# Kernel tuning notes

Measured on AMD Instinct MI355X. Metric: run time of the kernel, lower is better.

## Reference

```python
import jax, jax.numpy as jnp
import numpy as np

B, N, IN_F, OUT_F, REL_DIM, NUM_REL = 4, 2048, 256, 128, 10, 6
D = OUT_F // 2  # internal_dim
ALPHA = 0.2
LAMBDA_INIT = 0.8 - 0.6 * float(np.exp(-0.3 * 1))  # depth=1
EPS = 1e-5


def setup_inputs() -> dict:
    key = jax.random.key(0)
    ks = jax.random.split(key, 16)
    return {
        "h": jax.random.normal(ks[0], (B, N, IN_F), jnp.float32),
        "adj": jax.random.randint(ks[1], (B, N, N), 0, NUM_REL, jnp.int32),
        "W": jax.random.normal(ks[2], (IN_F, OUT_F), jnp.float32) * (1.414 / np.sqrt(IN_F)),
        "a_left_pos": jax.random.normal(ks[3], (D,), jnp.float32) * 0.1,
        "a_right_pos": jax.random.normal(ks[4], (D,), jnp.float32) * 0.1,
        "a_left_neg": jax.random.normal(ks[5], (D,), jnp.float32) * 0.1,
        "a_right_neg": jax.random.normal(ks[6], (D,), jnp.float32) * 0.1,
        "rel_emb": jax.random.normal(ks[7], (NUM_REL, REL_DIM), jnp.float32),
        "a_rel_pos": jax.random.normal(ks[8], (REL_DIM,), jnp.float32) * 0.3,
        "a_rel_neg": jax.random.normal(ks[9], (REL_DIM,), jnp.float32) * 0.3,
        "lambda_left1": jax.random.normal(ks[10], (D,), jnp.float32) * 0.1,
        "lambda_right1": jax.random.normal(ks[11], (D,), jnp.float32) * 0.1,
        "lambda_left2": jax.random.normal(ks[12], (D,), jnp.float32) * 0.1,
        "lambda_right2": jax.random.normal(ks[13], (D,), jnp.float32) * 0.1,
        "ln_gamma": jnp.ones((OUT_F,), jnp.float32),
        "ln_beta": jnp.zeros((OUT_F,), jnp.float32),
    }


def _leaky_relu(x):
    return jnp.where(x >= 0, x, ALPHA * x)


def reference(h, adj, W, a_left_pos, a_right_pos, a_left_neg, a_right_neg,
              rel_emb, a_rel_pos, a_rel_neg,
              lambda_left1, lambda_right1, lambda_left2, lambda_right2,
              ln_gamma, ln_beta):
    Wh = jnp.einsum('bnf,fo->bno', h, W)              # [B,N,OUT_F]
    Wh4 = Wh.reshape(B, N, 2, D)
    Wh_pos, Wh_neg = Wh4[:, :, 0, :], Wh4[:, :, 1, :]  # [B,N,D]

    # e[b,i,j] = left[b,i] + right[b,j] + rel_score[adj[b,i,j]]
    # relation Linear(rel_dim,1) applied to embedding rows == per-relation scalar lookup
    rel_score_pos = rel_emb @ a_rel_pos               # [NUM_REL]
    rel_score_neg = rel_emb @ a_rel_neg
    e_pos = (Wh_pos @ a_left_pos)[:, :, None] + (Wh_pos @ a_right_pos)[:, None, :] + rel_score_pos[adj]
    e_neg = (Wh_neg @ a_left_neg)[:, :, None] + (Wh_neg @ a_right_neg)[:, None, :] + rel_score_neg[adj]

    neg_inf = jnp.float32(-9e15)
    mask = adj > 0
    attn_pos = jax.nn.softmax(jnp.where(mask, _leaky_relu(e_pos), neg_inf), axis=2)
    attn_neg = jax.nn.softmax(jnp.where(mask, _leaky_relu(e_neg), neg_inf), axis=2)

    lam1 = jnp.exp(jnp.sum(lambda_left1 * lambda_right1))
    lam2 = jnp.exp(jnp.sum(lambda_left2 * lambda_right2))
    lambda_full = lam1 - lam2 + LAMBDA_INIT
    attention = attn_pos - lambda_full * attn_neg     # [B,N,N]

    Wh_v = jnp.concatenate([Wh_pos, Wh_neg], axis=-1)  # [B,N,OUT_F]
    h_prime = jnp.einsum('bij,bjo->bio', attention, Wh_v)

    mu = jnp.mean(h_prime, axis=-1, keepdims=True)
    var = jnp.mean(jnp.square(h_prime - mu), axis=-1, keepdims=True)
    h_prime = (h_prime - mu) * jax.lax.rsqrt(var + EPS) * ln_gamma + ln_beta
    h_prime = h_prime * (1.0 - LAMBDA_INIT)
    return jax.nn.gelu(h_prime, approximate=False), attention
```

## Files before the change

### kernel.cpp

```cpp
#include <hip/hip_runtime.h>
#include <math.h>

typedef short bf16x8 __attribute__((ext_vector_type(8)));
typedef float f32x4  __attribute__((ext_vector_type(4)));

constexpr int   B_    = 4;
constexpr int   N_    = 2048;
constexpr int   INF_  = 256;
constexpr int   OUTF_ = 128;
constexpr float LAMBDA_INIT_ = 0.35550906759096926f;
constexpr float OUT_SCALE_   = 0.64449093240903074f;
constexpr float EPS_         = 1e-5f;
constexpr float LOG2E_       = 1.44269504088896340736f;

__device__ inline unsigned short f2bf(float x) {
  unsigned u = __float_as_uint(x);
  u += 0x7fffu + ((u >> 16) & 1u);
  return (unsigned short)(u >> 16);
}
__device__ inline unsigned pack2(float a, float b) {
  return (unsigned)f2bf(a) | ((unsigned)f2bf(b) << 16);
}

__global__ void scalars_kernel(const float* __restrict__ rel_emb,
                               const float* __restrict__ a_rel_pos,
                               const float* __restrict__ a_rel_neg,
                               const float* __restrict__ ll1, const float* __restrict__ lr1,
                               const float* __restrict__ ll2, const float* __restrict__ lr2,
                               float* __restrict__ scal) {
  int lane = threadIdx.x;
  float p1 = ll1[lane] * lr1[lane];
  float p2 = ll2[lane] * lr2[lane];
  #pragma unroll
  for (int off = 32; off; off >>= 1) { p1 += __shfl_xor(p1, off); p2 += __shfl_xor(p2, off); }
  if (lane == 0) scal[12] = expf(p1) - expf(p2) + LAMBDA_INIT_;
  if (lane < 6) {
    float sp = 0.f, sn = 0.f;
    for (int k = 0; k < 10; ++k) {
      float rv = rel_emb[lane * 10 + k];
      sp += rv * a_rel_pos[k];
      sn += rv * a_rel_neg[k];
    }
    scal[lane]     = sp * LOG2E_;
    scal[6 + lane] = sn * LOG2E_;
  }
}

__global__ __launch_bounds__(256) void wh_dots_kernel(
    const float* __restrict__ h, const float* __restrict__ W,
    const float* __restrict__ alp, const float* __restrict__ arp,
    const float* __restrict__ aln, const float* __restrict__ arn,
    unsigned short* __restrict__ WhvT,
    float* __restrict__ lposv, float* __restrict__ rposv,
    float* __restrict__ lnegv, float* __restrict__ rnegv) {
  __shared__ __align__(16) float hT[INF_][20];
  const int t = threadIdx.x;
  const size_t row0 = (size_t)blockIdx.x * 16;
  #pragma unroll
  for (int i = 0; i < 16; ++i) hT[t][i] = h[(row0 + i) * INF_ + t];
  __syncthreads();
  const int c  = t & 127;
  const int rg = t >> 7;
  float acc[8] = {0.f, 0.f, 0.f, 0.f, 0.f, 0.f, 0.f, 0.f};
  #pragma unroll 4
  for (int k = 0; k < INF_; ++k) {
    float wv = W[k * OUTF_ + c];
    const float4* hp = reinterpret_cast<const float4*>(&hT[k][rg * 8]);
    float4 h0 = hp[0], h1 = hp[1];
    acc[0] += h0.x * wv; acc[1] += h0.y * wv; acc[2] += h0.z * wv; acc[3] += h0.w * wv;
    acc[4] += h1.x * wv; acc[5] += h1.y * wv; acc[6] += h1.z * wv; acc[7] += h1.w * wv;
  }
  uint4 pk;
  pk.x = pack2(acc[0], acc[1]); pk.y = pack2(acc[2], acc[3]);
  pk.z = pack2(acc[4], acc[5]); pk.w = pack2(acc[6], acc[7]);
  const int b  = (int)(row0 >> 11);
  const int n0 = (int)(row0 & 2047) + rg * 8;
  *reinterpret_cast<uint4*>(WhvT + ((size_t)b * OUTF_ + c) * N_ + n0) = pk;

  const int lane = t & 63;
  const int wv   = t >> 6;
  const bool pos = (wv & 1) == 0;
  const float al = pos ? alp[lane] : aln[lane];
  const float ar = pos ? arp[lane] : arn[lane];
  float sl[8], sr2[8];
  #pragma unroll
  for (int r = 0; r < 8; ++r) { sl[r] = acc[r] * al; sr2[r] = acc[r] * ar; }
  #pragma unroll
  for (int off = 32; off; off >>= 1) {
    #pragma unroll
    for (int r = 0; r < 8; ++r) {
      sl[r]  += __shfl_xor(sl[r],  off);
      sr2[r] += __shfl_xor(sr2[r], off);
    }
  }
  if (lane == 0) {
    #pragma unroll
    for (int r = 0; r < 8; ++r) {
      const int node = (int)row0 + rg * 8 + r;
      if (pos) { lposv[node] = sl[r] * LOG2E_; rposv[node] = sr2[r] * LOG2E_; }
      else     { lnegv[node] = sl[r] * LOG2E_; rnegv[node] = sr2[r] * LOG2E_; }
    }
  }
}

__global__ __launch_bounds__(512, 4) void fused_attn_pv(
    const int* __restrict__ adj,
    const float* __restrict__ lposv, const float* __restrict__ rposv,
    const float* __restrict__ lnegv, const float* __restrict__ rnegv,
    const float* __restrict__ scal, const unsigned short* __restrict__ WhvT,
    const float* __restrict__ gamma, const float* __restrict__ beta,
    float* __restrict__ out0, float* __restrict__ out1) {
  __shared__ __align__(16) uint4 A4[16 * 256];
  float* scr = reinterpret_cast<float*>(&A4[15 * 256]);
  float (*hp)[132] = reinterpret_cast<float (*)[132]>(A4);

  const int t = threadIdx.x;
  const int lane = t & 63;
  const int wv = t >> 6;
  const int bi = blockIdx.x;
  const int b  = bi >> 7;
  const int i0 = (bi & 127) * 16;
  const int flat0 = b * N_ + i0;

  const float lam = scal[12];
  float srcP = -1.0e30f, srcN = -1.0e30f;
  if (lane >= 1 && lane <= 5) { srcP = scal[lane]; srcN = scal[6 + lane]; }
  const int iSrcP = __float_as_int(srcP);
  const int iSrcN = __float_as_int(srcN);

  const int j0 = t * 4;
  float4 rp4 = *reinterpret_cast<const float4*>(rposv + b * N_ + j0);
  float4 rn4 = *reinterpret_cast<const float4*>(rnegv + b * N_ + j0);
  const float rp[4] = {rp4.x, rp4.y, rp4.z, rp4.w};
  const float rn[4] = {rn4.x, rn4.y, rn4.z, rn4.w};

  const int wchunk = (t >> 1) >> 5;
  const int wloc   = (t >> 1) & 31;

  int4 avN = *reinterpret_cast<const int4*>(adj + (size_t)flat0 * N_ + j0);

  for (int r = 0; r < 16; ++r) {
    const int flat = flat0 + r;
    const int4 av4 = avN;
    if (r < 15)
      avN = *reinterpret_cast<const int4*>(adj + (size_t)(flat + 1) * N_ + j0);
    const float lP = lposv[flat];
    const float lN = lnegv[flat];
    int av[4] = {av4.x, av4.y, av4.z, av4.w};

    float p[4], n[4];
    #pragma unroll
    for (int q = 0; q < 4; ++q) {
      float rsp = __int_as_float(__builtin_amdgcn_ds_bpermute(av[q] << 2, iSrcP));
      float rsn = __int_as_float(__builtin_amdgcn_ds_bpermute(av[q] << 2, iSrcN));
      float e  = lP + rp[q] + rsp;
      float en = lN + rn[q] + rsn;
      e  = fmaxf(e, 0.2f * e);
      en = fmaxf(en, 0.2f * en);
      p[q] = __builtin_amdgcn_exp2f(e);
      n[q] = __builtin_amdgcn_exp2f(en);
    }
    float sP = (p[0] + p[1]) + (p[2] + p[3]);
    float sN = (n[0] + n[1]) + (n[2] + n[3]);
    #pragma unroll
    for (int off = 32; off; off >>= 1) { sP += __shfl_xor(sP, off); sN += __shfl_xor(sN, off); }
    const int bf = r & 1;
    if (lane == 0) { scr[bf * 16 + wv] = sP; scr[bf * 16 + 8 + wv] = sN; }
    __syncthreads();
    float vP = scr[bf * 16 + (lane & 7)];
    vP += __shfl_xor(vP, 1); vP += __shfl_xor(vP, 2); vP += __shfl_xor(vP, 4);
    float vN = scr[bf * 16 + 8 + (lane & 7)];
    vN += __shfl_xor(vN, 1); vN += __shfl_xor(vN, 2); vN += __shfl_xor(vN, 4);
    const float s1 = 1.f / vP;
    const float s2 = -lam / vN;

    float a[4];
    #pragma unroll
    for (int q = 0; q < 4; ++q) a[q] = p[q] * s1 + n[q] * s2;
    float* o1 = out1 + (size_t)flat * N_ + j0;
    *reinterpret_cast<float4*>(o1) = make_float4(a[0], a[1], a[2], a[3]);

    if (r == 15) __syncthreads();
    const int uidx = r * 256 + wchunk * 32 + (wloc ^ (r & 7));
    uint2 val;
    val.x = pack2(a[0], a[1]); val.y = pack2(a[2], a[3]);
    reinterpret_cast<uint2*>(A4)[uidx * 2 + (t & 1)] = val;
  }
  __syncthreads();

  const int bl  = lane & 15;
  const int kg  = lane >> 4;
  const int ch  = wv * 16 + bl;
  const unsigned short* Bp = WhvT + ((size_t)b * OUTF_ + ch) * N_ + kg * 8;
  f32x4 acc0 = {0.f, 0.f, 0.f, 0.f};
  f32x4 acc1 = {0.f, 0.f, 0.f, 0.f};
  const int arow = bl * 256;
  const int aswz = bl & 7;

  bf16x8 bBuf[2][8];
  #pragma unroll
  for (int kk = 0; kk < 8; ++kk)
    bBuf[0][kk] = *reinterpret_cast<const bf16x8*>(Bp + kk * 32);

  #pragma unroll
  for (int c = 0; c < 8; ++c) {
    const int cur = c & 1;
    if (c < 7) {
      #pragma unroll
      for (int kk = 0; kk < 8; ++kk)
        bBuf[cur ^ 1][kk] = *reinterpret_cast<const bf16x8*>(Bp + (c + 1) * 256 + kk * 32);
    }
    #pragma unroll
    for (int kk = 0; kk < 8; ++kk) {
      bf16x8 a = *reinterpret_cast<const bf16x8*>(&A4[arow + c * 32 + ((kk * 4 + kg) ^ aswz)]);
      if (cur == 0) acc0 = __builtin_amdgcn_mfma_f32_16x16x32_bf16(a, bBuf[0][kk], acc0, 0, 0, 0);
      else          acc1 = __builtin_amdgcn_mfma_f32_16x16x32_bf16(a, bBuf[1][kk], acc1, 0, 0, 0);
    }
  }
  __syncthreads();

  #pragma unroll
  for (int q = 0; q < 4; ++q) hp[kg * 4 + q][ch] = acc0[q] + acc1[q];
  __syncthreads();

  const int row = t >> 5;
  const int c0  = t & 31;
  float v[4], s = 0.f, sq = 0.f;
  #pragma unroll
  for (int e = 0; e < 4; ++e) {
    v[e] = hp[row][c0 + e * 32];
    s += v[e]; sq += v[e] * v[e];
  }
  #pragma unroll
  for (int off = 16; off; off >>= 1) { s += __shfl_xor(s, off); sq += __shfl_xor(sq, off); }
  const float mu  = s  * (1.f / 128.f);
  const float var = sq * (1.f / 128.f) - mu * mu;
  const float inv = rsqrtf(var + EPS_);
  float* orow = out0 + ((size_t)(b * N_ + i0 + row)) * OUTF_;
  #pragma unroll
  for (int e = 0; e < 4; ++e) {
    const int chh = c0 + e * 32;
    float y = (v[e] - mu) * inv * gamma[chh] + beta[chh];
    y *= OUT_SCALE_;
    orow[chh] = 0.5f * y * (1.f + erff(y * 0.70710678118654752f));
  }
}

extern "C" void kernel_launch(void* const* d_in, const int* in_sizes, int n_in,
                              void* d_out, int out_size, void* d_ws, size_t ws_size,
                              hipStream_t stream) {
  (void)in_sizes; (void)n_in; (void)out_size; (void)ws_size;
  const float* h        = (const float*)d_in[0];
  const int*   adj      = (const int*)d_in[1];
  const float* W        = (const float*)d_in[2];
  const float* alp      = (const float*)d_in[3];
  const float* arp      = (const float*)d_in[4];
  const float* aln      = (const float*)d_in[5];
  const float* arn      = (const float*)d_in[6];
  const float* rel_emb  = (const float*)d_in[7];
  const float* a_rel_p  = (const float*)d_in[8];
  const float* a_rel_n  = (const float*)d_in[9];
  const float* ll1      = (const float*)d_in[10];
  const float* lr1      = (const float*)d_in[11];
  const float* ll2      = (const float*)d_in[12];
  const float* lr2      = (const float*)d_in[13];
  const float* gamma    = (const float*)d_in[14];
  const float* beta     = (const float*)d_in[15];

  float* out0 = (float*)d_out;
  float* out1 = out0 + (size_t)B_ * N_ * OUTF_;

  float* ws    = (float*)d_ws;
  float* scal  = ws;
  float* lposv = ws + 32;
  float* rposv = lposv + B_ * N_;
  float* lnegv = rposv + B_ * N_;
  float* rnegv = lnegv + B_ * N_;
  unsigned short* WhvT = (unsigned short*)(rnegv + B_ * N_);

  scalars_kernel<<<1, 64, 0, stream>>>(rel_emb, a_rel_p, a_rel_n, ll1, lr1, ll2, lr2, scal);
  wh_dots_kernel<<<(B_ * N_) / 16, 256, 0, stream>>>(h, W, alp, arp, aln, arn,
                                                     WhvT, lposv, rposv, lnegv, rnegv);
  fused_attn_pv<<<B_ * (N_ / 16), 512, 0, stream>>>(adj, lposv, rposv, lnegv, rnegv,
                                                    scal, WhvT, gamma, beta, out0, out1);
}
```

Before: 89.39 us.

## Retile Wh projection kernel to 4x4 register blocking over 32-row tiles

Rewrites the h·W projection kernel so each block handles 32 rows and each thread computes a 4-row by 4-column register tile, loading W and h as float4 vectors. This raises arithmetic intensity and cuts per-FMA shared-memory and global load traffic compared with the previous one-column, eight-row scheme. The attention-vector dot products are now reduced over 16-lane groups rather than full waves. The grid is halved, so fewer blocks are available to fill the GPU, and the kernel is a small part of total time next to the attention kernel.

Measured after the change: 81.97 us. 1.09x faster.

```diff
diff --git a/kernel.cpp b/kernel.cpp
--- a/kernel.cpp
+++ b/kernel.cpp
@@ -46,59 +46,93 @@
   }
 }
 
-__global__ __launch_bounds__(256) void wh_dots_kernel(
+__global__ __launch_bounds__(256) void wh_dots_v2(
     const float* __restrict__ h, const float* __restrict__ W,
     const float* __restrict__ alp, const float* __restrict__ arp,
     const float* __restrict__ aln, const float* __restrict__ arn,
     unsigned short* __restrict__ WhvT,
     float* __restrict__ lposv, float* __restrict__ rposv,
     float* __restrict__ lnegv, float* __restrict__ rnegv) {
-  __shared__ __align__(16) float hT[INF_][20];
+  __shared__ __align__(16) float hT[32][260];
   const int t = threadIdx.x;
-  const size_t row0 = (size_t)blockIdx.x * 16;
-  #pragma unroll
-  for (int i = 0; i < 16; ++i) hT[t][i] = h[(row0 + i) * INF_ + t];
+  const int row0 = blockIdx.x * 32;
+  const int b = row0 >> 11;
+
+  #pragma unroll 8
+  for (int i = 0; i < 32; ++i) hT[i][t] = h[(size_t)(row0 + i) * INF_ + t];
   __syncthreads();
-  const int c  = t & 127;
-  const int rg = t >> 7;
-  float acc[8] = {0.f, 0.f, 0.f, 0.f, 0.f, 0.f, 0.f, 0.f};
-  #pragma unroll 4
-  for (int k = 0; k < INF_; ++k) {
-    float wv = W[k * OUTF_ + c];
-    const float4* hp = reinterpret_cast<const float4*>(&hT[k][rg * 8]);
-    float4 h0 = hp[0], h1 = hp[1];
-    acc[0] += h0.x * wv; acc[1] += h0.y * wv; acc[2] += h0.z * wv; acc[3] += h0.w * wv;
-    acc[4] += h1.x * wv; acc[5] += h1.y * wv; acc[6] += h1.z * wv; acc[7] += h1.w * wv;
-  }
-  uint4 pk;
-  pk.x = pack2(acc[0], acc[1]); pk.y = pack2(acc[2], acc[3]);
-  pk.z = pack2(acc[4], acc[5]); pk.w = pack2(acc[6], acc[7]);
-  const int b  = (int)(row0 >> 11);
-  const int n0 = (int)(row0 & 2047) + rg * 8;
-  *reinterpret_cast<uint4*>(WhvT + ((size_t)b * OUTF_ + c) * N_ + n0) = pk;
-
-  const int lane = t & 63;
-  const int wv   = t >> 6;
-  const bool pos = (wv & 1) == 0;
-  const float al = pos ? alp[lane] : aln[lane];
-  const float ar = pos ? arp[lane] : arn[lane];
-  float sl[8], sr2[8];
-  #pragma unroll
-  for (int r = 0; r < 8; ++r) { sl[r] = acc[r] * al; sr2[r] = acc[r] * ar; }
-  #pragma unroll
-  for (int off = 32; off; off >>= 1) {
-    #pragma unroll
-    for (int r = 0; r < 8; ++r) {
-      sl[r]  += __shfl_xor(sl[r],  off);
-      sr2[r] += __shfl_xor(sr2[r], off);
-    }
-  }
-  if (lane == 0) {
-    #pragma unroll
-    for (int r = 0; r < 8; ++r) {
-      const int node = (int)row0 + rg * 8 + r;
-      if (pos) { lposv[node] = sl[r] * LOG2E_; rposv[node] = sr2[r] * LOG2E_; }
-      else     { lnegv[node] = sl[r] * LOG2E_; rnegv[node] = sr2[r] * LOG2E_; }
+
+  const int rg = t >> 5;
+  const int cg = t & 31;
+  const int c0 = cg * 4;
+  float acc[4][4] = {{0.f,0.f,0.f,0.f},{0.f,0.f,0.f,0.f},{0.f,0.f,0.f,0.f},{0.f,0.f,0.f,0.f}};
+
+  #pragma unroll 2
+  for (int k4 = 0; k4 < 64; ++k4) {
+    float4 hv[4], wv[4];
+    #pragma unroll
+    for (int rr = 0; rr < 4; ++rr)
+      hv[rr] = *reinterpret_cast<const float4*>(&hT[rg * 4 + rr][k4 * 4]);
+    #pragma unroll
+    for (int j = 0; j < 4; ++j)
+      wv[j] = *reinterpret_cast<const float4*>(&W[(size_t)(k4 * 4 + j) * OUTF_ + c0]);
+    #pragma unroll
+    for (int rr = 0; rr < 4; ++rr) {
+      const float* hp = reinterpret_cast<const float*>(&hv[rr]);
+      #pragma unroll
+      for (int j = 0; j < 4; ++j) {
+        const float* wp = reinterpret_cast<const float*>(&wv[j]);
+        acc[rr][0] += hp[j] * wp[0];
+        acc[rr][1] += hp[j] * wp[1];
+        acc[rr][2] += hp[j] * wp[2];
+        acc[rr][3] += hp[j] * wp[3];
+      }
+    }
+  }
+
+  const int n0 = (row0 & 2047) + rg * 4;
+  #pragma unroll
+  for (int cc = 0; cc < 4; ++cc) {
+    uint2 v;
+    v.x = pack2(acc[0][cc], acc[1][cc]);
+    v.y = pack2(acc[2][cc], acc[3][cc]);
+    *reinterpret_cast<uint2*>(WhvT + ((size_t)b * OUTF_ + c0 + cc) * N_ + n0) = v;
+  }
+
+  float aL[4], aR[4];
+  #pragma unroll
+  for (int cc = 0; cc < 4; ++cc) {
+    const int c = c0 + cc;
+    aL[cc] = (c < 64) ? alp[c] : aln[c - 64];
+    aR[cc] = (c < 64) ? arp[c] : arn[c - 64];
+  }
+  float sl[4], sr2[4];
+  #pragma unroll
+  for (int rr = 0; rr < 4; ++rr) {
+    sl[rr]  = (acc[rr][0] * aL[0] + acc[rr][1] * aL[1]) + (acc[rr][2] * aL[2] + acc[rr][3] * aL[3]);
+    sr2[rr] = (acc[rr][0] * aR[0] + acc[rr][1] * aR[1]) + (acc[rr][2] * aR[2] + acc[rr][3] * aR[3]);
+  }
+  #pragma unroll
+  for (int off = 1; off <= 8; off <<= 1) {
+    #pragma unroll
+    for (int rr = 0; rr < 4; ++rr) {
+      sl[rr]  += __shfl_xor(sl[rr],  off);
+      sr2[rr] += __shfl_xor(sr2[rr], off);
+    }
+  }
+  if (cg == 0) {
+    #pragma unroll
+    for (int rr = 0; rr < 4; ++rr) {
+      const int node = row0 + rg * 4 + rr;
+      lposv[node] = sl[rr]  * LOG2E_;
+      rposv[node] = sr2[rr] * LOG2E_;
+    }
+  } else if (cg == 16) {
+    #pragma unroll
+    for (int rr = 0; rr < 4; ++rr) {
+      const int node = row0 + rg * 4 + rr;
+      lnegv[node] = sl[rr]  * LOG2E_;
+      rnegv[node] = sr2[rr] * LOG2E_;
     }
   }
 }
@@ -279,8 +313,8 @@
   unsigned short* WhvT = (unsigned short*)(rnegv + B_ * N_);
 
   scalars_kernel<<<1, 64, 0, stream>>>(rel_emb, a_rel_p, a_rel_n, ll1, lr1, ll2, lr2, scal);
-  wh_dots_kernel<<<(B_ * N_) / 16, 256, 0, stream>>>(h, W, alp, arp, aln, arn,
-                                                     WhvT, lposv, rposv, lnegv, rnegv);
+  wh_dots_v2<<<(B_ * N_) / 32, 256, 0, stream>>>(h, W, alp, arp, aln, arn,
+                                                 WhvT, lposv, rposv, lnegv, rnegv);
   fused_attn_pv<<<B_ * (N_ / 16), 512, 0, stream>>>(adj, lposv, rposv, lnegv, rnegv,
                                                     scal, WhvT, gamma, beta, out0, out1);
 }
```
